# Kernel tuning notes

Hardware: AMD Instinct MI355X
Metric: run time of the kernel (lower is better)

The kernel has to match this reference:

```python
import jax, jax.numpy as jnp
import numpy as np

# LIF-with-refractory parameters (match init_kwargs)
DT = 1e-3
TAU_MEM_INV = 100.0     # 1/tau_mem
TAU_SYN_INV = 200.0     # 1/tau_syn
TAU_REFRAC_INV = 1000.0 # 1/tau_refrac
V_TH = 1.0
V_LEAK = 0.0
V_RESET = 0.0
RHO_RESET = 5.0


def setup_inputs() -> dict:
    key = jax.random.key(0)
    k = jax.random.split(key, 6)
    B, C, H, W = 16, 32, 64, 64
    T_BUF = 64
    i_new = jax.random.normal(k[0], (B, C, H, W), dtype=jnp.float32)
    v = jax.random.uniform(k[1], (B, C, H, W), dtype=jnp.float32)
    i = jax.random.normal(k[2], (B, C, H, W), dtype=jnp.float32)
    rho = jax.random.uniform(k[3], (B, C, H, W), dtype=jnp.float32)
    buffer = jax.random.uniform(k[4], (T_BUF, B, C, H, W), dtype=jnp.float32)
    delay_idx = jax.random.randint(k[5], (B, C, H, W), 0, T_BUF, dtype=jnp.int32)
    return {"i_new": i_new, "v": v, "i": i, "rho": rho,
            "buffer": buffer, "delay_idx": delay_idx}


def reference(i_new, v, i, rho, buffer, delay_idx):
    """One Euler step of the modified LIF neuron with absolute refractory
    period and per-neuron delay-line gather (NT variant).

    dv   = dt/tau_mem * (1 - Theta(rho)) * (v_leak - v + i)
    di   = -dt/tau_syn * i            (then input current i_new is injected)
    drho = -dt/tau_refrac * Theta(rho)
    z    = Theta(v - v_th); v -> (1-z) v + z v_reset; rho -> rho + z rho_reset
    Output spikes are read from the delay buffer at per-neuron delays.
    Returns stacked [5, B, C, H, W]: (z_delayed, z, v_new, i_new_state, rho_new).
    """
    dtype = v.dtype
    refrac = (rho > 0).astype(dtype)                     # Theta(rho): in refractory
    # membrane integration, gated off while refractory
    v_dec = v + DT * TAU_MEM_INV * (1.0 - refrac) * (V_LEAK - v + i)
    # synaptic current decay + injected input
    i_dec = i - DT * TAU_SYN_INV * i + i_new
    # spike condition + reset transition
    z = (v_dec > V_TH).astype(dtype)
    v_new = (1.0 - z) * v_dec + z * V_RESET
    # refractory variable: decay while active, jump to rho_reset on spike
    rho_new = rho - DT * TAU_REFRAC_INV * refrac + z * RHO_RESET
    # push new spikes into the delay line (deque appendleft + pop)
    buffer_new = jnp.concatenate([z[None], buffer[:-1]], axis=0)  # [T,B,C,H,W]
    # per-neuron delayed spike gather along time axis
    z_delayed = jnp.take_along_axis(
        buffer_new, delay_idx[None].astype(jnp.int32), axis=0)[0]  # [B,C,H,W]
    return jnp.stack([z_delayed, z, v_new, i_dec, rho_new], axis=0)
```

## Files before the change

### kernel.cpp

```cpp
#include <hip/hip_runtime.h>
#include <hip/hip_bf16.h>


__global__ __launch_bounds__(256) void lif_step_kernel(
    const float4* __restrict__ i_new4,
    const float4* __restrict__ v4,
    const float4* __restrict__ i4,
    const float4* __restrict__ rho4,
    const float*  __restrict__ buffer,
    const int4*   __restrict__ delay4,
    float* __restrict__ out,
    int n8, int N)
{
    #pragma clang fp contract(off)

    int t = blockIdx.x * blockDim.x + threadIdx.x;
    if (t >= n8) return;

    int g  = t << 1;
    int n0 = t << 3;

    float4 vinA = v4[g],     vinB = v4[g + 1];
    float4 iinA = i4[g],     iinB = i4[g + 1];
    float4 rinA = rho4[g],   rinB = rho4[g + 1];
    float4 nA   = i_new4[g], nB   = i_new4[g + 1];
    int4   dlA  = delay4[g], dlB  = delay4[g + 1];

    const float vv[8] = {vinA.x, vinA.y, vinA.z, vinA.w, vinB.x, vinB.y, vinB.z, vinB.w};
    const float ii[8] = {iinA.x, iinA.y, iinA.z, iinA.w, iinB.x, iinB.y, iinB.z, iinB.w};
    const float rr[8] = {rinA.x, rinA.y, rinA.z, rinA.w, rinB.x, rinB.y, rinB.z, rinB.w};
    const float nn[8] = {nA.x,   nA.y,   nA.z,   nA.w,   nB.x,   nB.y,   nB.z,   nB.w};
    const int   dd[8] = {dlA.x,  dlA.y,  dlA.z,  dlA.w,  dlB.x,  dlB.y,  dlB.z,  dlB.w};

    float gbuf[8];
    #pragma unroll
    for (int j = 0; j < 8; ++j) {
        int d   = dd[j];
        int row = (d > 0) ? (d - 1) : 0;
        gbuf[j] = buffer[(size_t)((unsigned)row * (unsigned)N + (unsigned)(n0 + j))];
    }

    float z[8], vnew[8], idec[8], rnew[8], zdel[8];
    #pragma unroll
    for (int j = 0; j < 8; ++j) {
        float refrac = (rr[j] > 0.0f) ? 1.0f : 0.0f;
        float v_dec  = vv[j] + 0.1f * ((1.0f - refrac) * ((0.0f - vv[j]) + ii[j]));
        float zz     = (v_dec > 1.0f) ? 1.0f : 0.0f;
        z[j]    = zz;
        vnew[j] = (1.0f - zz) * v_dec;
        idec[j] = (ii[j] - 0.2f * ii[j]) + nn[j];
        rnew[j] = (rr[j] - refrac) + zz * 5.0f;
        zdel[j] = (dd[j] == 0) ? zz : gbuf[j];
    }

    float4* o0 = (float4*)(out + 0 * (size_t)N);
    float4* o1 = (float4*)(out + 1 * (size_t)N);
    float4* o2 = (float4*)(out + 2 * (size_t)N);
    float4* o3 = (float4*)(out + 3 * (size_t)N);
    float4* o4 = (float4*)(out + 4 * (size_t)N);

    o0[g]     = make_float4(zdel[0], zdel[1], zdel[2], zdel[3]);
    o0[g + 1] = make_float4(zdel[4], zdel[5], zdel[6], zdel[7]);
    o1[g]     = make_float4(z[0], z[1], z[2], z[3]);
    o1[g + 1] = make_float4(z[4], z[5], z[6], z[7]);
    o2[g]     = make_float4(vnew[0], vnew[1], vnew[2], vnew[3]);
    o2[g + 1] = make_float4(vnew[4], vnew[5], vnew[6], vnew[7]);
    o3[g]     = make_float4(idec[0], idec[1], idec[2], idec[3]);
    o3[g + 1] = make_float4(idec[4], idec[5], idec[6], idec[7]);
    o4[g]     = make_float4(rnew[0], rnew[1], rnew[2], rnew[3]);
    o4[g + 1] = make_float4(rnew[4], rnew[5], rnew[6], rnew[7]);
}

extern "C" void kernel_launch(void* const* d_in, const int* in_sizes, int n_in,
                              void* d_out, int out_size, void* d_ws, size_t ws_size,
                              hipStream_t stream) {
    const float* i_new  = (const float*)d_in[0];
    const float* v      = (const float*)d_in[1];
    const float* i_cur  = (const float*)d_in[2];
    const float* rho    = (const float*)d_in[3];
    const float* buffer = (const float*)d_in[4];
    const int*   delay  = (const int*)d_in[5];
    float* out = (float*)d_out;

    int N  = in_sizes[0];
    int n8 = N >> 3;

    int block = 256;
    int grid  = (n8 + block - 1) / block;

    lif_step_kernel<<<grid, block, 0, stream>>>(
        (const float4*)i_new, (const float4*)v, (const float4*)i_cur,
        (const float4*)rho, buffer, (const int4*)delay, out, n8, N);
}
```

Measured before the change: 657.8 us.

## Replace random delay-buffer gather with coalesced full-row streaming and select

Instead of gathering one scattered float per neuron from the delay buffer, each thread streams all 63 relevant buffer rows with coalesced float4 loads and selects the value matching each lane's delay. Work per thread also drops from 8 to 4 elements. This trades many uncoalesced partial-line accesses for reading the whole buffer sequentially, relying on the random delays already forcing most lines to be fetched. It adds compute and fixed bandwidth independent of the delay distribution.

```diff
diff --git a/kernel.cpp b/kernel.cpp
--- a/kernel.cpp
+++ b/kernel.cpp
@@ -1,5 +1,4 @@
 #include <hip/hip_runtime.h>
-#include <hip/hip_bf16.h>
 
 
 __global__ __launch_bounds__(256) void lif_step_kernel(
@@ -7,42 +6,31 @@
     const float4* __restrict__ v4,
     const float4* __restrict__ i4,
     const float4* __restrict__ rho4,
-    const float*  __restrict__ buffer,
+    const float4* __restrict__ buffer4,
     const int4*   __restrict__ delay4,
     float* __restrict__ out,
-    int n8, int N)
+    int n4)
 {
     #pragma clang fp contract(off)
 
     int t = blockIdx.x * blockDim.x + threadIdx.x;
-    if (t >= n8) return;
+    if (t >= n4) return;
 
-    int g  = t << 1;
-    int n0 = t << 3;
+    float4 vin = v4[t];
+    float4 iin = i4[t];
+    float4 rin = rho4[t];
+    float4 nin = i_new4[t];
+    int4   dl  = delay4[t];
 
-    float4 vinA = v4[g],     vinB = v4[g + 1];
-    float4 iinA = i4[g],     iinB = i4[g + 1];
-    float4 rinA = rho4[g],   rinB = rho4[g + 1];
-    float4 nA   = i_new4[g], nB   = i_new4[g + 1];
-    int4   dlA  = delay4[g], dlB  = delay4[g + 1];
+    const float vv[4] = {vin.x, vin.y, vin.z, vin.w};
+    const float ii[4] = {iin.x, iin.y, iin.z, iin.w};
+    const float rr[4] = {rin.x, rin.y, rin.z, rin.w};
+    const float nn[4] = {nin.x, nin.y, nin.z, nin.w};
+    const int   dd[4] = {dl.x, dl.y, dl.z, dl.w};
 
-    const float vv[8] = {vinA.x, vinA.y, vinA.z, vinA.w, vinB.x, vinB.y, vinB.z, vinB.w};
-    const float ii[8] = {iinA.x, iinA.y, iinA.z, iinA.w, iinB.x, iinB.y, iinB.z, iinB.w};
-    const float rr[8] = {rinA.x, rinA.y, rinA.z, rinA.w, rinB.x, rinB.y, rinB.z, rinB.w};
-    const float nn[8] = {nA.x,   nA.y,   nA.z,   nA.w,   nB.x,   nB.y,   nB.z,   nB.w};
-    const int   dd[8] = {dlA.x,  dlA.y,  dlA.z,  dlA.w,  dlB.x,  dlB.y,  dlB.z,  dlB.w};
-
-    float gbuf[8];
+    float z[4], vnew[4], idec[4], rnew[4];
     #pragma unroll
-    for (int j = 0; j < 8; ++j) {
-        int d   = dd[j];
-        int row = (d > 0) ? (d - 1) : 0;
-        gbuf[j] = buffer[(size_t)((unsigned)row * (unsigned)N + (unsigned)(n0 + j))];
-    }
-
-    float z[8], vnew[8], idec[8], rnew[8], zdel[8];
-    #pragma unroll
-    for (int j = 0; j < 8; ++j) {
+    for (int j = 0; j < 4; ++j) {
         float refrac = (rr[j] > 0.0f) ? 1.0f : 0.0f;
         float v_dec  = vv[j] + 0.1f * ((1.0f - refrac) * ((0.0f - vv[j]) + ii[j]));
         float zz     = (v_dec > 1.0f) ? 1.0f : 0.0f;
@@ -50,25 +38,36 @@
         vnew[j] = (1.0f - zz) * v_dec;
         idec[j] = (ii[j] - 0.2f * ii[j]) + nn[j];
         rnew[j] = (rr[j] - refrac) + zz * 5.0f;
-        zdel[j] = (dd[j] == 0) ? zz : gbuf[j];
     }
 
-    float4* o0 = (float4*)(out + 0 * (size_t)N);
-    float4* o1 = (float4*)(out + 1 * (size_t)N);
-    float4* o2 = (float4*)(out + 2 * (size_t)N);
-    float4* o3 = (float4*)(out + 3 * (size_t)N);
-    float4* o4 = (float4*)(out + 4 * (size_t)N);
+    const unsigned r0 = (unsigned)dd[0] - 1u;
+    const unsigned r1 = (unsigned)dd[1] - 1u;
+    const unsigned r2 = (unsigned)dd[2] - 1u;
+    const unsigned r3 = (unsigned)dd[3] - 1u;
+    float zd0 = 0.0f, zd1 = 0.0f, zd2 = 0.0f, zd3 = 0.0f;
 
-    o0[g]     = make_float4(zdel[0], zdel[1], zdel[2], zdel[3]);
-    o0[g + 1] = make_float4(zdel[4], zdel[5], zdel[6], zdel[7]);
-    o1[g]     = make_float4(z[0], z[1], z[2], z[3]);
-    o1[g + 1] = make_float4(z[4], z[5], z[6], z[7]);
-    o2[g]     = make_float4(vnew[0], vnew[1], vnew[2], vnew[3]);
-    o2[g + 1] = make_float4(vnew[4], vnew[5], vnew[6], vnew[7]);
-    o3[g]     = make_float4(idec[0], idec[1], idec[2], idec[3]);
-    o3[g + 1] = make_float4(idec[4], idec[5], idec[6], idec[7]);
-    o4[g]     = make_float4(rnew[0], rnew[1], rnew[2], rnew[3]);
-    o4[g + 1] = make_float4(rnew[4], rnew[5], rnew[6], rnew[7]);
+    const float4* bp = buffer4 + t;
+    #pragma unroll 7
+    for (unsigned r = 0; r < 63u; ++r) {
+        float4 bv = *bp;
+        bp += n4;
+        zd0 = (r == r0) ? bv.x : zd0;
+        zd1 = (r == r1) ? bv.y : zd1;
+        zd2 = (r == r2) ? bv.z : zd2;
+        zd3 = (r == r3) ? bv.w : zd3;
+    }
+    zd0 = (dd[0] == 0) ? z[0] : zd0;
+    zd1 = (dd[1] == 0) ? z[1] : zd1;
+    zd2 = (dd[2] == 0) ? z[2] : zd2;
+    zd3 = (dd[3] == 0) ? z[3] : zd3;
+
+    float4* o = (float4*)out;
+    size_t  s = (size_t)n4;
+    o[0 * s + t] = make_float4(zd0, zd1, zd2, zd3);
+    o[1 * s + t] = make_float4(z[0], z[1], z[2], z[3]);
+    o[2 * s + t] = make_float4(vnew[0], vnew[1], vnew[2], vnew[3]);
+    o[3 * s + t] = make_float4(idec[0], idec[1], idec[2], idec[3]);
+    o[4 * s + t] = make_float4(rnew[0], rnew[1], rnew[2], rnew[3]);
 }
 
 extern "C" void kernel_launch(void* const* d_in, const int* in_sizes, int n_in,
@@ -83,12 +82,13 @@
     float* out = (float*)d_out;
 
     int N  = in_sizes[0];
-    int n8 = N >> 3;
+    int n4 = N >> 2;
 
     int block = 256;
-    int grid  = (n8 + block - 1) / block;
+    int grid  = (n4 + block - 1) / block;
 
     lif_step_kernel<<<grid, block, 0, stream>>>(
         (const float4*)i_new, (const float4*)v, (const float4*)i_cur,
-        (const float4*)rho, buffer, (const int4*)delay, out, n8, N);
+        (const float4*)rho, (const float4*)buffer, (const int4*)delay,
+        out, n4);
 }
```

Result: slower. 731.6 us (+11.2%).
